# Kernel optimization log

Measured on AMD Instinct MI355X. Metric: run time of the kernel, lower is better.

The kernel has to match this reference:

```python
import jax, jax.numpy as jnp
import numpy as np

B, S, D = 4, 2048, 1024
EPS = 1e-5


def setup_inputs() -> dict:
    key = jax.random.key(0)
    ks = jax.random.split(key, 8)
    s = 1.0 / np.sqrt(D)
    return {
        "x": jax.random.normal(ks[0], (B, S, D), dtype=jnp.float32),
        "Wq": jax.random.normal(ks[1], (D, D), dtype=jnp.float32) * s,
        "Wk": jax.random.normal(ks[2], (D, D), dtype=jnp.float32) * s,
        "Wv": jax.random.normal(ks[3], (D, D), dtype=jnp.float32) * s,
        "W1": jax.random.normal(ks[4], (D, D), dtype=jnp.float32) * s,
        "b1": jnp.zeros((D,), dtype=jnp.float32),
        "W2": jax.random.normal(ks[5], (D, D), dtype=jnp.float32) * s,
        "b2": jnp.zeros((D,), dtype=jnp.float32),
        "gamma": jnp.ones((D,), dtype=jnp.float32),
        "beta": jnp.zeros((D,), dtype=jnp.float32),
    }


def _layer_norm(x, gamma, beta):
    mu = jnp.mean(x, axis=-1, keepdims=True)
    var = jnp.mean(jnp.square(x - mu), axis=-1, keepdims=True)
    return (x - mu) * jax.lax.rsqrt(var + EPS) * gamma + beta


def reference(x, Wq, Wk, Wv, W1, b1, W2, b2, gamma, beta):
    seq_len, d = x.shape[1], x.shape[2]
    # torch Linear: y = x @ W.T
    Q = jnp.einsum('bsd,ed->bse', x, Wq)
    K = jnp.einsum('bsd,ed->bse', x, Wk)
    V = jnp.einsum('bsd,ed,->bse', x, Wv, jnp.float32(1.0)) if False else jnp.einsum('bsd,ed->bse', x, Wv)
    scores = jnp.einsum('bqd,bkd->bqk', Q, K) / jnp.sqrt(jnp.float32(d))
    causal = jnp.tril(jnp.ones((seq_len, seq_len), dtype=bool))  # [S,S]
    scores = jnp.where(causal[None, :, :], scores, -jnp.inf)
    attn = jax.nn.softmax(scores, axis=-1)
    attn_out = jnp.einsum('bqk,bkd->bqd', attn, V)
    # dropout is identity at eval
    h = _layer_norm(x + attn_out, gamma, beta)
    ff = jnp.einsum('bsd,ed->bse', jax.nn.relu(jnp.einsum('bsd,ed->bse', h, W1) + b1), W2) + b2
    out = _layer_norm(h + ff, gamma, beta)
    return out
```

## Files before the change

### kernel.cpp

```cpp
#include <hip/hip_runtime.h>
#include <math.h>
#include <cstdint>
#include <cstddef>

#define DI __device__ __forceinline__

typedef __bf16 bf16x8 __attribute__((ext_vector_type(8)));
typedef float f32x4 __attribute__((ext_vector_type(4)));

static constexpr int kB = 4, kS = 2048, kD = 1024;
static constexpr int kM = kB * kS;
static constexpr float kScale = 0.03125f;
static constexpr float kEps = 1e-5f;

DI unsigned short f2bf(float f) {
  unsigned u = __float_as_uint(f);
  u += 0x7FFFu + ((u >> 16) & 1u);
  return (unsigned short)(u >> 16);
}
DI float bf2f(unsigned short h) {
  return __uint_as_float(((unsigned)h) << 16);
}

DI void gld_lds16(const void* g, void* l) {
  __builtin_amdgcn_global_load_lds(
      (__attribute__((address_space(1))) void*)(void*)g,
      (__attribute__((address_space(3))) void*)l, 16, 0, 0);
}

#define SBAR() __builtin_amdgcn_sched_barrier(0)
#define FULLBAR() do { SBAR(); __builtin_amdgcn_s_barrier(); SBAR(); } while (0)

__global__ __launch_bounds__(256) void k_cast_all(
    const float* __restrict__ x, const float* __restrict__ Wq,
    const float* __restrict__ Wk, const float* __restrict__ Wv,
    const float* __restrict__ W1, const float* __restrict__ W2,
    unsigned short* __restrict__ xb, unsigned short* __restrict__ Wqkb,
    unsigned short* __restrict__ Wvb, unsigned short* __restrict__ W1b,
    unsigned short* __restrict__ W2b) {
  const int i = blockIdx.x * 256 + threadIdx.x;
  const int X4 = kM * kD / 4;
  const int W4 = kD * kD / 4;
  const float* src;
  unsigned short* dst;
  int j;
  if (i < X4) { src = x; dst = xb; j = i; }
  else if (i < X4 + W4)     { src = Wq; dst = Wqkb;          j = i - X4; }
  else if (i < X4 + 2 * W4) { src = Wk; dst = Wqkb + 4 * W4; j = i - X4 - W4; }
  else if (i < X4 + 3 * W4) { src = Wv; dst = Wvb;           j = i - X4 - 2 * W4; }
  else if (i < X4 + 4 * W4) { src = W1; dst = W1b;           j = i - X4 - 3 * W4; }
  else                      { src = W2; dst = W2b;           j = i - X4 - 4 * W4; }
  float4 v = ((const float4*)src)[j];
  ushort4 o;
  o.x = f2bf(v.x); o.y = f2bf(v.y); o.z = f2bf(v.z); o.w = f2bf(v.w);
  ((ushort4*)dst)[j] = o;
}

template <int NF, int OUT_BF16, int RELU>
__global__ __launch_bounds__(512, 2) void k_gemm8p(
    const unsigned short* __restrict__ A, const unsigned short* __restrict__ B,
    void* __restrict__ Cv, const float* __restrict__ bias,
    int M, int N, int K, int lda, int ldb, int ldc,
    long sA, long sB, long sC, int cColOff) {
  constexpr int BN = NF * 64;
  constexpr int LB = BN / 128;
  constexpr int VM = 2 + 2 * LB;
  constexpr int AH = 256 * 32;
  constexpr int BH = BN * 32;

  int lin = blockIdx.x + gridDim.x * blockIdx.y;
  const int nblk = gridDim.x * gridDim.y;
  if ((nblk & 7) == 0)
    lin = (lin & 7) * (nblk >> 3) + (lin >> 3);
  const int bm = (lin / gridDim.x) * 256;
  const int bn = (lin % gridDim.x) * BN;
  A += (long)blockIdx.z * sA;
  B += (long)blockIdx.z * sB;

  const int tid = threadIdx.x;
  const int lane = tid & 63;
  const int wm = (tid >> 6) >> 2;
  const int wn = (tid >> 6) & 3;
  const int fm = lane & 15;
  const int fq = lane >> 4;

  __shared__ __align__(16) unsigned short Asm[2 * 2 * AH];
  __shared__ __align__(16) unsigned short Bsm[2 * 2 * BH];

  long aoff[2];
#pragma unroll
  for (int i = 0; i < 2; ++i) {
    const int ci = i * 512 + tid;
    const int row = ci >> 2;
    const int g = (ci & 3) ^ ((row >> 1) & 3);
    aoff[i] = (long)(bm + row) * lda + g * 8;
  }
  long boff[LB];
#pragma unroll
  for (int i = 0; i < LB; ++i) {
    const int ci = i * 512 + tid;
    const int row = ci >> 2;
    const int g = (ci & 3) ^ ((row >> 1) & 3);
    boff[i] = (long)(bn + row) * ldb + g * 8;
  }

  const int NT = K >> 6;

  auto stA = [&](int d, int kh, int t) {
    const unsigned short* s = A + t * 64 + kh * 32;
    unsigned short* dst = Asm + (d * 2 + kh) * AH;
#pragma unroll
    for (int i = 0; i < 2; ++i)
      gld_lds16(s + aoff[i], dst + (i * 512 + tid) * 8);
  };
  auto stB = [&](int d, int kh, int t) {
    const unsigned short* s = B + t * 64 + kh * 32;
    unsigned short* dst = Bsm + (d * 2 + kh) * BH;
#pragma unroll
    for (int i = 0; i < LB; ++i)
      gld_lds16(s + boff[i], dst + (i * 512 + tid) * 8);
  };

  const int slotoff = (fq ^ ((fm >> 1) & 3)) * 8;
  const unsigned short* aRd = Asm + (wm * 128 + fm) * 32 + slotoff;
  const unsigned short* bRd = Bsm + (wn * (NF * 16) + fm) * 32 + slotoff;

  f32x4 acc[8][NF];
#pragma unroll
  for (int m = 0; m < 8; ++m)
#pragma unroll
    for (int n = 0; n < NF; ++n) acc[m][n] = (f32x4){0.f, 0.f, 0.f, 0.f};

  stB(0, 0, 0); stA(0, 0, 0); stB(0, 1, 0); stA(0, 1, 0);
  if (NT > 1) { stB(1, 0, 1); stA(1, 0, 1); stB(1, 1, 1); }
  SBAR();
  asm volatile("s_waitcnt vmcnt(%0)" :: "i"(VM) : "memory");
  __builtin_amdgcn_s_barrier();
  SBAR();

  bf16x8 af[4], bfr[NF];

  for (int t = 0; t < NT; ++t) {
    const int d = t & 1;
    const unsigned short* aB0 = aRd + d * (2 * AH);
    const unsigned short* bB0 = bRd + d * (2 * BH);
    const unsigned short* aB1 = aB0 + AH;
    const unsigned short* bB1 = bB0 + BH;

#pragma unroll
    for (int m = 0; m < 4; ++m) af[m] = *(const bf16x8*)(aB0 + m * 512);
#pragma unroll
    for (int n = 0; n < NF; ++n) bfr[n] = *(const bf16x8*)(bB0 + n * 512);
    if (t + 1 < NT) stA(d ^ 1, 1, t + 1);
    FULLBAR();
    __builtin_amdgcn_s_setprio(1);
#pragma unroll
    for (int m = 0; m < 4; ++m)
#pragma unroll
      for (int n = 0; n < NF; ++n)
        acc[m][n] = __builtin_amdgcn_mfma_f32_16x16x32_bf16(af[m], bfr[n], acc[m][n], 0, 0, 0);
    __builtin_amdgcn_s_setprio(0);
    FULLBAR();

#pragma unroll
    for (int m = 0; m < 4; ++m) af[m] = *(const bf16x8*)(aB0 + (4 + m) * 512);
    if (t + 2 < NT) stB(d, 0, t + 2);
    FULLBAR();
    __builtin_amdgcn_s_setprio(1);
#pragma unroll
    for (int m = 0; m < 4; ++m)
#pragma unroll
      for (int n = 0; n < NF; ++n)
        acc[4 + m][n] = __builtin_amdgcn_mfma_f32_16x16x32_bf16(af[m], bfr[n], acc[4 + m][n], 0, 0, 0);
    __builtin_amdgcn_s_setprio(0);
    FULLBAR();

#pragma unroll
    for (int m = 0; m < 4; ++m) af[m] = *(const bf16x8*)(aB1 + m * 512);
#pragma unroll
    for (int n = 0; n < NF; ++n) bfr[n] = *(const bf16x8*)(bB1 + n * 512);
    if (t + 2 < NT) stA(d, 0, t + 2);
    FULLBAR();
    __builtin_amdgcn_s_setprio(1);
#pragma unroll
    for (int m = 0; m < 4; ++m)
#pragma unroll
      for (int n = 0; n < NF; ++n)
        acc[m][n] = __builtin_amdgcn_mfma_f32_16x16x32_bf16(af[m], bfr[n], acc[m][n], 0, 0, 0);
    __builtin_amdgcn_s_setprio(0);
    FULLBAR();

#pragma unroll
    for (int m = 0; m < 4; ++m) af[m] = *(const bf16x8*)(aB1 + (4 + m) * 512);
    if (t + 2 < NT) stB(d, 1, t + 2);
    SBAR();
    if (t < NT - 2)
      asm volatile("s_waitcnt vmcnt(%0)" :: "i"(VM) : "memory");
    else
      asm volatile("s_waitcnt vmcnt(0)" ::: "memory");
    __builtin_amdgcn_s_barrier();
    SBAR();
    __builtin_amdgcn_s_setprio(1);
#pragma unroll
    for (int m = 0; m < 4; ++m)
#pragma unroll
      for (int n = 0; n < NF; ++n)
        acc[4 + m][n] = __builtin_amdgcn_mfma_f32_16x16x32_bf16(af[m], bfr[n], acc[4 + m][n], 0, 0, 0);
    __builtin_amdgcn_s_setprio(0);
    FULLBAR();
  }

  const long cb = (long)blockIdx.z * sC;
  float bv[NF];
#pragma unroll
  for (int n = 0; n < NF; ++n)
    bv[n] = bias ? bias[bn + wn * (NF * 16) + n * 16 + fm] : 0.f;
#pragma unroll
  for (int m = 0; m < 8; ++m) {
#pragma unroll
    for (int r = 0; r < 4; ++r) {
      const int row = bm + wm * 128 + m * 16 + fq * 4 + r;
#pragma unroll
      for (int n = 0; n < NF; ++n) {
        const int col = cColOff + bn + wn * (NF * 16) + n * 16 + fm;
        float v = acc[m][n][r] + bv[n];
        if (RELU) v = fmaxf(v, 0.f);
        if (OUT_BF16)
          ((unsigned short*)Cv)[cb + (long)row * ldc + col] = f2bf(v);
        else
          ((float*)Cv)[cb + (long)row * ldc + col] = v;
      }
    }
  }
}

template <int OUT_BF16, int RELU, int CAUSAL>
__global__ __launch_bounds__(256, 2) void k_gemm_nt(
    const unsigned short* __restrict__ A, const unsigned short* __restrict__ B,
    void* __restrict__ Cv, const float* __restrict__ bias,
    int M, int N, int K, int lda, int ldb, int ldc,
    long sA, long sB, long sC) {
  int bm, bn;
  {
    int lin = blockIdx.x + gridDim.x * blockIdx.y;
    const int nblk = gridDim.x * gridDim.y;
    if ((nblk & 7) == 0)
      lin = (lin & 7) * (nblk >> 3) + (lin >> 3);
    if (CAUSAL == 1) {
      const int t = lin;
      int r = (int)floorf((sqrtf(8.f * (float)t + 1.f) - 1.f) * 0.5f);
      while ((r + 1) * (r + 2) / 2 <= t) ++r;
      while (r * (r + 1) / 2 > t) --r;
      bm = r * 128;
      bn = (t - r * (r + 1) / 2) * 128;
    } else {
      bm = (lin / gridDim.x) * 128;
      bn = (lin % gridDim.x) * 128;
    }
  }
  A += (long)blockIdx.z * sA;
  B += (long)blockIdx.z * sB;

  const int tid = threadIdx.x;
  const int lane = tid & 63;
  const int wm = ((tid >> 6) >> 1) * 64;
  const int wn = ((tid >> 6) & 1) * 64;

  __shared__ __align__(16) unsigned short Asm[128 * 64];
  __shared__ __align__(16) unsigned short Bsm[128 * 64];

  f32x4 acc[4][4];
#pragma unroll
  for (int i = 0; i < 4; ++i)
#pragma unroll
    for (int j = 0; j < 4; ++j) acc[i][j] = (f32x4){0.f, 0.f, 0.f, 0.f};

  const int r_row = tid >> 3;
  const int dst_k = (tid & 7) * 8;
  const int src_k = ((tid & 7) ^ ((tid >> 3) & 7)) * 8;
  const int fm = lane & 15;
  const int fq = lane >> 4;

  for (int k0 = 0; k0 < K; k0 += 64) {
#pragma unroll
    for (int i = 0; i < 4; ++i) {
      const int row = i * 32 + r_row;
      gld_lds16(A + (long)(bm + row) * lda + (k0 + src_k), Asm + row * 64 + dst_k);
      gld_lds16(B + (long)(bn + row) * ldb + (k0 + src_k), Bsm + row * 64 + dst_k);
    }
    __syncthreads();
#pragma unroll
    for (int kk = 0; kk < 2; ++kk) {
      bf16x8 af[4], bfr[4];
#pragma unroll
      for (int i = 0; i < 4; ++i) {
        const int pa = ((kk * 4 + fq) ^ (fm & 7)) * 8;
        af[i]  = *(const bf16x8*)(Asm + (wm + i * 16 + fm) * 64 + pa);
        bfr[i] = *(const bf16x8*)(Bsm + (wn + i * 16 + fm) * 64 + pa);
      }
#pragma unroll
      for (int i = 0; i < 4; ++i)
#pragma unroll
        for (int j = 0; j < 4; ++j)
          acc[i][j] = __builtin_amdgcn_mfma_f32_16x16x32_bf16(af[i], bfr[j], acc[i][j], 0, 0, 0);
    }
    __syncthreads();
  }

  const long cb = (long)blockIdx.z * sC;
#pragma unroll
  for (int i = 0; i < 4; ++i) {
#pragma unroll
    for (int j = 0; j < 4; ++j) {
      const int col = bn + wn + j * 16 + fm;
      const float bv = bias ? bias[col] : 0.f;
#pragma unroll
      for (int r = 0; r < 4; ++r) {
        const int row = bm + wm + i * 16 + fq * 4 + r;
        float v = acc[i][j][r] + bv;
        if (RELU) v = fmaxf(v, 0.f);
        if (OUT_BF16)
          ((unsigned short*)Cv)[cb + (long)row * ldc + col] = f2bf(v);
        else
          ((float*)Cv)[cb + (long)row * ldc + col] = v;
      }
    }
  }
}

__global__ __launch_bounds__(256, 2) void k_attn_pv(
    const unsigned short* __restrict__ P, const unsigned short* __restrict__ Vt,
    unsigned short* __restrict__ O) {
  const int r = blockIdx.x;
  const int q = blockIdx.y + 16 * blockIdx.z;
  const int lx = q & 7;
  const int pq = r + 8 * (q >> 3);
  const int pair = pq & 15;
  const int zz = pq >> 4;

  const int bn = lx * 128;
  const int bm_hi = (31 - pair) * 64;
  const int bm_lo = pair * 64;
  const int Khi = bm_hi + 64;
  const int Klo = bm_lo + 64;
  P  += (long)zz * kS * kS;
  Vt += (long)zz * kD * kS;
  O  += (long)zz * kS * kD;

  const int tid = threadIdx.x;
  const int lane = tid & 63;
  const int wn = (tid >> 6) * 32;

  __shared__ __align__(16) unsigned short Ah[64 * 64];
  __shared__ __align__(16) unsigned short Al[64 * 64];
  __shared__ __align__(16) unsigned short Bs[128 * 64];

  f32x4 ah[4][2], al[4][2];
#pragma unroll
  for (int i = 0; i < 4; ++i)
#pragma unroll
    for (int j = 0; j < 2; ++j) {
      ah[i][j] = (f32x4){0.f, 0.f, 0.f, 0.f};
      al[i][j] = (f32x4){0.f, 0.f, 0.f, 0.f};
    }

  const int r_row = tid >> 3;
  const int dst_k = (tid & 7) * 8;
  const int src_k = ((tid & 7) ^ ((tid >> 3) & 7)) * 8;
  const int fm = lane & 15;
  const int fq = lane >> 4;

  for (int k0 = 0; k0 < Khi; k0 += 64) {
    const bool lo = (k0 < Klo);
#pragma unroll
    for (int i = 0; i < 2; ++i) {
      const int row = i * 32 + r_row;
      gld_lds16(P + (long)(bm_hi + row) * kS + (k0 + src_k), Ah + row * 64 + dst_k);
      if (lo)
        gld_lds16(P + (long)(bm_lo + row) * kS + (k0 + src_k), Al + row * 64 + dst_k);
    }
#pragma unroll
    for (int i = 0; i < 4; ++i) {
      const int row = i * 32 + r_row;
      gld_lds16(Vt + (long)(bn + row) * kS + (k0 + src_k), Bs + row * 64 + dst_k);
    }
    __syncthreads();
#pragma unroll
    for (int kk = 0; kk < 2; ++kk) {
      bf16x8 afh[4], afl[4], bfr[2];
#pragma unroll
      for (int i = 0; i < 4; ++i) {
        const int ra = i * 16 + fm;
        const int pa = ((kk * 4 + fq) ^ (ra & 7)) * 8;
        afh[i] = *(const bf16x8*)(Ah + ra * 64 + pa);
        afl[i] = *(const bf16x8*)(Al + ra * 64 + pa);
      }
#pragma unroll
      for (int j = 0; j < 2; ++j) {
        const int rb = wn + j * 16 + fm;
        const int pb = ((kk * 4 + fq) ^ (rb & 7)) * 8;
        bfr[j] = *(const bf16x8*)(Bs + rb * 64 + pb);
      }
#pragma unroll
      for (int i = 0; i < 4; ++i)
#pragma unroll
        for (int j = 0; j < 2; ++j)
          ah[i][j] = __builtin_amdgcn_mfma_f32_16x16x32_bf16(afh[i], bfr[j], ah[i][j], 0, 0, 0);
      if (lo) {
#pragma unroll
        for (int i = 0; i < 4; ++i)
#pragma unroll
          for (int j = 0; j < 2; ++j)
            al[i][j] = __builtin_amdgcn_mfma_f32_16x16x32_bf16(afl[i], bfr[j], al[i][j], 0, 0, 0);
      }
    }
    __syncthreads();
  }

#pragma unroll
  for (int i = 0; i < 4; ++i) {
#pragma unroll
    for (int j = 0; j < 2; ++j) {
      const int col = bn + wn + j * 16 + fm;
#pragma unroll
      for (int r2 = 0; r2 < 4; ++r2) {
        const int rr = i * 16 + fq * 4 + r2;
        O[(long)(bm_hi + rr) * kD + col] = f2bf(ah[i][j][r2]);
        O[(long)(bm_lo + rr) * kD + col] = f2bf(al[i][j][r2]);
      }
    }
  }
}

DI float wsum(float v) {
  v += __shfl_xor(v, 32, 64);
  v += __shfl_xor(v, 16, 64);
  v += __shfl_xor(v, 8, 64);
  v += __shfl_xor(v, 4, 64);
  v += __shfl_xor(v, 2, 64);
  v += __shfl_xor(v, 1, 64);
  return v;
}
DI float wmax(float v) {
  v = fmaxf(v, __shfl_xor(v, 32, 64));
  v = fmaxf(v, __shfl_xor(v, 16, 64));
  v = fmaxf(v, __shfl_xor(v, 8, 64));
  v = fmaxf(v, __shfl_xor(v, 4, 64));
  v = fmaxf(v, __shfl_xor(v, 2, 64));
  v = fmaxf(v, __shfl_xor(v, 1, 64));
  return v;
}

__global__ __launch_bounds__(256) void k_softmax_causal(
    const unsigned short* __restrict__ S, unsigned short* __restrict__ P) {
  const int row = blockIdx.x;
  const int q = row & (kS - 1);
  const int lim = (q & ~127) + 128;
  const unsigned short* Srow = S + (long)row * kS;
  unsigned short* Prow = P + (long)row * kS;
  const int tid = threadIdx.x;
  __shared__ float red[4];

  float v[8];
  float mx = -INFINITY;
#pragma unroll
  for (int i = 0; i < 8; ++i) {
    const int k = tid + i * 256;
    float xv = -INFINITY;
    if (k <= q) xv = bf2f(Srow[k]) * kScale;
    v[i] = xv;
    mx = fmaxf(mx, xv);
  }
  mx = wmax(mx);
  if ((tid & 63) == 0) red[tid >> 6] = mx;
  __syncthreads();
  mx = fmaxf(fmaxf(red[0], red[1]), fmaxf(red[2], red[3]));
  __syncthreads();

  float sum = 0.f;
#pragma unroll
  for (int i = 0; i < 8; ++i) {
    const float e = (v[i] > -INFINITY) ? __expf(v[i] - mx) : 0.f;
    v[i] = e;
    sum += e;
  }
  sum = wsum(sum);
  if ((tid & 63) == 0) red[tid >> 6] = sum;
  __syncthreads();
  sum = red[0] + red[1] + red[2] + red[3];
  const float inv = 1.f / sum;
#pragma unroll
  for (int i = 0; i < 8; ++i) {
    const int k = tid + i * 256;
    if (k < lim) Prow[k] = f2bf(v[i] * inv);
  }
}

template <int X_BF16, int OUT_FP32>
__global__ __launch_bounds__(256) void k_residual_ln(
    const void* __restrict__ Xv, const unsigned short* __restrict__ Yb,
    const float* __restrict__ gamma, const float* __restrict__ beta,
    float* __restrict__ Out, unsigned short* __restrict__ OutB) {
  const long base = (long)blockIdx.x * kD;
  const int tid = threadIdx.x;
  __shared__ float reds[4], redss[4];
  float v[4];
  float s = 0.f, ss2 = 0.f;
#pragma unroll
  for (int i = 0; i < 4; ++i) {
    const int k = tid + i * 256;
    const float xf = X_BF16 ? bf2f(((const unsigned short*)Xv)[base + k])
                            : ((const float*)Xv)[base + k];
    const float xv = xf + bf2f(Yb[base + k]);
    v[i] = xv;
    s += xv;
    ss2 += xv * xv;
  }
  s = wsum(s);
  ss2 = wsum(ss2);
  if ((tid & 63) == 0) { reds[tid >> 6] = s; redss[tid >> 6] = ss2; }
  __syncthreads();
  s = reds[0] + reds[1] + reds[2] + reds[3];
  ss2 = redss[0] + redss[1] + redss[2] + redss[3];
  const float mu = s * (1.f / kD);
  float var = ss2 * (1.f / kD) - mu * mu;
  var = fmaxf(var, 0.f);
  const float rstd = rsqrtf(var + kEps);
#pragma unroll
  for (int i = 0; i < 4; ++i) {
    const int k = tid + i * 256;
    const float y = (v[i] - mu) * rstd * gamma[k] + beta[k];
    if (OUT_FP32) Out[base + k] = y;
    else          OutB[base + k] = f2bf(y);
  }
}

extern "C" void kernel_launch(void* const* d_in, const int* in_sizes, int n_in,
                              void* d_out, int out_size, void* d_ws, size_t ws_size,
                              hipStream_t stream) {
  (void)in_sizes; (void)n_in; (void)out_size; (void)ws_size;
  const float* x     = (const float*)d_in[0];
  const float* Wq    = (const float*)d_in[1];
  const float* Wk    = (const float*)d_in[2];
  const float* Wv    = (const float*)d_in[3];
  const float* W1    = (const float*)d_in[4];
  const float* b1    = (const float*)d_in[5];
  const float* W2    = (const float*)d_in[6];
  const float* b2    = (const float*)d_in[7];
  const float* gamma = (const float*)d_in[8];
  const float* beta  = (const float*)d_in[9];
  float* out = (float*)d_out;

  char* base = (char*)d_ws;
  size_t off = 0;
  auto alloc = [&](size_t bytes) -> void* {
    void* p = base + off;
    off = (off + bytes + 255) & ~(size_t)255;
    return p;
  };

  unsigned short* xb     = (unsigned short*)alloc((size_t)kM * kD * 2);
  unsigned short* Wqkb   = (unsigned short*)alloc((size_t)2 * kD * kD * 2);
  unsigned short* Wvb    = (unsigned short*)alloc((size_t)kD * kD * 2);
  unsigned short* W1b    = (unsigned short*)alloc((size_t)kD * kD * 2);
  unsigned short* W2b    = (unsigned short*)alloc((size_t)kD * kD * 2);
  unsigned short* QKb    = (unsigned short*)alloc((size_t)kM * 2 * kD * 2);
  unsigned short* Vt     = (unsigned short*)alloc((size_t)kM * kD * 2);
  unsigned short* Sb     = (unsigned short*)alloc((size_t)kB * kS * kS * 2);
  unsigned short* Pb     = (unsigned short*)alloc((size_t)kB * kS * kS * 2);
  unsigned short* attn_b = (unsigned short*)alloc((size_t)kM * kD * 2);
  unsigned short* ff_b = attn_b;
  unsigned short* hb   = Sb;
  unsigned short* mid  = Pb;

  dim3 blk(256);
  dim3 blk8(512);

  {
    const int n4 = (kM * kD + 5 * kD * kD) / 4;
    k_cast_all<<<n4 / 256, blk, 0, stream>>>(x, Wq, Wk, Wv, W1, W2,
                                             xb, Wqkb, Wvb, W1b, W2b);
  }

  k_gemm_nt<1, 0, 0><<<dim3(2 * kD / 128, kM / 128, 1), blk, 0, stream>>>(
      xb, Wqkb, QKb, nullptr, kM, 2 * kD, kD, kD, kD, 2 * kD, 0, 0, 0);

  k_gemm8p<2, 1, 0><<<dim3(kS / 128, kD / 256, kB), blk8, 0, stream>>>(
      Wvb, xb, Vt, nullptr, kD, kS, kD, kD, kD, kS,
      0, (long)kS * kD, (long)kD * kS, 0);

  k_gemm_nt<1, 0, 1><<<dim3(136, 1, kB), blk, 0, stream>>>(
      QKb, QKb + kD, Sb, nullptr, kS, kS, kD, 2 * kD, 2 * kD, kS,
      (long)kS * 2 * kD, (long)kS * 2 * kD, (long)kS * kS);

  k_softmax_causal<<<kM, blk, 0, stream>>>(Sb, Pb);

  k_attn_pv<<<dim3(8, 16, kB), blk, 0, stream>>>(Pb, Vt, attn_b);

  k_residual_ln<0, 0><<<kM, blk, 0, stream>>>(x, attn_b, gamma, beta,
                                              nullptr, hb);

  k_gemm8p<2, 1, 1><<<dim3(kD / 128, kM / 256, 1), blk8, 0, stream>>>(
      hb, W1b, mid, b1, kM, kD, kD, kD, kD, kD, 0, 0, 0, 0);
  k_gemm8p<2, 1, 0><<<dim3(kD / 128, kM / 256, 1), blk8, 0, stream>>>(
      mid, W2b, ff_b, b2, kM, kD, kD, kD, kD, kD, 0, 0, 0, 0);

  k_residual_ln<1, 1><<<kM, blk, 0, stream>>>(hb, ff_b, gamma, beta,
                                              out, nullptr);
}
```

Baseline: 324.8 us.

## Replace paired-row attention PV kernel with causal-aware 128x128 GEMM tiles

```diff
diff --git a/kernel.cpp b/kernel.cpp
--- a/kernel.cpp
+++ b/kernel.cpp
@@ -241,25 +241,45 @@
     int M, int N, int K, int lda, int ldb, int ldc,
     long sA, long sB, long sC) {
   int bm, bn;
+  int Keff = K;
+  long cb;
   {
     int lin = blockIdx.x + gridDim.x * blockIdx.y;
-    const int nblk = gridDim.x * gridDim.y;
-    if ((nblk & 7) == 0)
-      lin = (lin & 7) * (nblk >> 3) + (lin >> 3);
-    if (CAUSAL == 1) {
-      const int t = lin;
-      int r = (int)floorf((sqrtf(8.f * (float)t + 1.f) - 1.f) * 0.5f);
-      while ((r + 1) * (r + 2) / 2 <= t) ++r;
-      while (r * (r + 1) / 2 > t) --r;
-      bm = r * 128;
-      bn = (t - r * (r + 1) / 2) * 128;
+    if (CAUSAL == 2) {
+      const int l = (lin & 7) * 64 + (lin >> 3);
+      const int x = l >> 6;
+      const int i = l & 63;
+      const int half = i >> 5;
+      const int j = i & 31;
+      const int qr = half ? x : 15 - x;
+      const int zz = (j >> 3) & 3;
+      const int dc = j & 7;
+      bm = qr * 128;
+      bn = dc * 128;
+      Keff = bm + 128;
+      A += (long)zz * sA;
+      B += (long)zz * sB;
+      cb = (long)zz * sC;
     } else {
-      bm = (lin / gridDim.x) * 128;
-      bn = (lin % gridDim.x) * 128;
+      const int nblk = gridDim.x * gridDim.y;
+      if ((nblk & 7) == 0)
+        lin = (lin & 7) * (nblk >> 3) + (lin >> 3);
+      if (CAUSAL == 1) {
+        const int t = lin;
+        int r = (int)floorf((sqrtf(8.f * (float)t + 1.f) - 1.f) * 0.5f);
+        while ((r + 1) * (r + 2) / 2 <= t) ++r;
+        while (r * (r + 1) / 2 > t) --r;
+        bm = r * 128;
+        bn = (t - r * (r + 1) / 2) * 128;
+      } else {
+        bm = (lin / gridDim.x) * 128;
+        bn = (lin % gridDim.x) * 128;
+      }
+      A += (long)blockIdx.z * sA;
+      B += (long)blockIdx.z * sB;
+      cb = (long)blockIdx.z * sC;
     }
   }
-  A += (long)blockIdx.z * sA;
-  B += (long)blockIdx.z * sB;
 
   const int tid = threadIdx.x;
   const int lane = tid & 63;
@@ -281,7 +301,7 @@
   const int fm = lane & 15;
   const int fq = lane >> 4;
 
-  for (int k0 = 0; k0 < K; k0 += 64) {
+  for (int k0 = 0; k0 < Keff; k0 += 64) {
 #pragma unroll
     for (int i = 0; i < 4; ++i) {
       const int row = i * 32 + r_row;
@@ -307,7 +327,6 @@
     __syncthreads();
   }
 
-  const long cb = (long)blockIdx.z * sC;
 #pragma unroll
   for (int i = 0; i < 4; ++i) {
 #pragma unroll
@@ -323,110 +342,6 @@
           ((unsigned short*)Cv)[cb + (long)row * ldc + col] = f2bf(v);
         else
           ((float*)Cv)[cb + (long)row * ldc + col] = v;
-      }
-    }
-  }
-}
-
-__global__ __launch_bounds__(256, 2) void k_attn_pv(
-    const unsigned short* __restrict__ P, const unsigned short* __restrict__ Vt,
-    unsigned short* __restrict__ O) {
-  const int r = blockIdx.x;
-  const int q = blockIdx.y + 16 * blockIdx.z;
-  const int lx = q & 7;
-  const int pq = r + 8 * (q >> 3);
-  const int pair = pq & 15;
-  const int zz = pq >> 4;
-
-  const int bn = lx * 128;
-  const int bm_hi = (31 - pair) * 64;
-  const int bm_lo = pair * 64;
-  const int Khi = bm_hi + 64;
-  const int Klo = bm_lo + 64;
-  P  += (long)zz * kS * kS;
-  Vt += (long)zz * kD * kS;
-  O  += (long)zz * kS * kD;
-
-  const int tid = threadIdx.x;
-  const int lane = tid & 63;
-  const int wn = (tid >> 6) * 32;
-
-  __shared__ __align__(16) unsigned short Ah[64 * 64];
-  __shared__ __align__(16) unsigned short Al[64 * 64];
-  __shared__ __align__(16) unsigned short Bs[128 * 64];
-
-  f32x4 ah[4][2], al[4][2];
-#pragma unroll
-  for (int i = 0; i < 4; ++i)
-#pragma unroll
-    for (int j = 0; j < 2; ++j) {
-      ah[i][j] = (f32x4){0.f, 0.f, 0.f, 0.f};
-      al[i][j] = (f32x4){0.f, 0.f, 0.f, 0.f};
-    }
-
-  const int r_row = tid >> 3;
-  const int dst_k = (tid & 7) * 8;
-  const int src_k = ((tid & 7) ^ ((tid >> 3) & 7)) * 8;
-  const int fm = lane & 15;
-  const int fq = lane >> 4;
-
-  for (int k0 = 0; k0 < Khi; k0 += 64) {
-    const bool lo = (k0 < Klo);
-#pragma unroll
-    for (int i = 0; i < 2; ++i) {
-      const int row = i * 32 + r_row;
-      gld_lds16(P + (long)(bm_hi + row) * kS + (k0 + src_k), Ah + row * 64 + dst_k);
-      if (lo)
-        gld_lds16(P + (long)(bm_lo + row) * kS + (k0 + src_k), Al + row * 64 + dst_k);
-    }
-#pragma unroll
-    for (int i = 0; i < 4; ++i) {
-      const int row = i * 32 + r_row;
-      gld_lds16(Vt + (long)(bn + row) * kS + (k0 + src_k), Bs + row * 64 + dst_k);
-    }
-    __syncthreads();
-#pragma unroll
-    for (int kk = 0; kk < 2; ++kk) {
-      bf16x8 afh[4], afl[4], bfr[2];
-#pragma unroll
-      for (int i = 0; i < 4; ++i) {
-        const int ra = i * 16 + fm;
-        const int pa = ((kk * 4 + fq) ^ (ra & 7)) * 8;
-        afh[i] = *(const bf16x8*)(Ah + ra * 64 + pa);
-        afl[i] = *(const bf16x8*)(Al + ra * 64 + pa);
-      }
-#pragma unroll
-      for (int j = 0; j < 2; ++j) {
-        const int rb = wn + j * 16 + fm;
-        const int pb = ((kk * 4 + fq) ^ (rb & 7)) * 8;
-        bfr[j] = *(const bf16x8*)(Bs + rb * 64 + pb);
-      }
-#pragma unroll
-      for (int i = 0; i < 4; ++i)
-#pragma unroll
-        for (int j = 0; j < 2; ++j)
-          ah[i][j] = __builtin_amdgcn_mfma_f32_16x16x32_bf16(afh[i], bfr[j], ah[i][j], 0, 0, 0);
-      if (lo) {
-#pragma unroll
-        for (int i = 0; i < 4; ++i)
-#pragma unroll
-          for (int j = 0; j < 2; ++j)
-            al[i][j] = __builtin_amdgcn_mfma_f32_16x16x32_bf16(afl[i], bfr[j], al[i][j], 0, 0, 0);
-      }
-    }
-    __syncthreads();
-  }
-
-#pragma unroll
-  for (int i = 0; i < 4; ++i) {
-#pragma unroll
-    for (int j = 0; j < 2; ++j) {
-      const int col = bn + wn + j * 16 + fm;
-#pragma unroll
-      for (int r2 = 0; r2 < 4; ++r2) {
-        const int rr = i * 16 + fq * 4 + r2;
-        O[(long)(bm_hi + rr) * kD + col] = f2bf(ah[i][j][r2]);
-        O[(long)(bm_lo + rr) * kD + col] = f2bf(al[i][j][r2]);
       }
     }
   }
@@ -595,7 +510,9 @@
 
   k_softmax_causal<<<kM, blk, 0, stream>>>(Sb, Pb);
 
-  k_attn_pv<<<dim3(8, 16, kB), blk, 0, stream>>>(Pb, Vt, attn_b);
+  k_gemm_nt<1, 0, 2><<<dim3(8, 64, 1), blk, 0, stream>>>(
+      Pb, Vt, attn_b, nullptr, kS, kD, 0, kS, kS, kD,
+      (long)kS * kS, (long)kD * kS, (long)kS * kD);
 
   k_residual_ln<0, 0><<<kM, blk, 0, stream>>>(x, attn_b, gamma, beta,
                                               nullptr, hb);
```

Result: slower. 339.4 us (+4.5%).
